# Optimization experiments

Hardware: AMD Instinct MI355X
Metric: run time of the kernel (lower is better)

Reference implementation:

```python
import jax, jax.numpy as jnp
import numpy as np

NEG_SLOPE = 0.2   # opt.alpha for LeakyReLU
NEG_INF = -9e15   # mask fill used by LocalAggregator

B, L, D, V = 512, 100, 128, 200000


def setup_inputs() -> dict:
    key = jax.random.key(0)
    ks = jax.random.split(key, 6)
    stdv = 1.0 / np.sqrt(D)
    inputs = jax.random.randint(ks[0], (B, L), 0, V)
    adj = jax.random.randint(ks[1], (B, L, L), 0, 5)        # edge types 0..4
    mask_item = jax.random.randint(ks[2], (B, L), 0, 2)
    item = jax.random.randint(ks[3], (B, L), 0, V)
    emb_table = jax.random.uniform(ks[4], (V, D), jnp.float32, -stdv, stdv)
    ka = jax.random.split(ks[5], 4)
    a0, a1, a2, a3 = [jax.random.uniform(k, (D,), jnp.float32, -stdv, stdv) for k in ka]
    return dict(inputs=inputs, adj=adj, mask_item=mask_item, item=item,
                emb_table=emb_table, a0=a0, a1=a1, a2=a2, a3=a3)


def reference(inputs, adj, mask_item, item, emb_table, a0, a1, a2, a3):
    # h = self.embedding(inputs)
    h = emb_table[inputs]  # [B, L, D]

    # LocalAggregator (GCE-GNN): a_input[b,i,j,:] = h[b,i,:] * h[b,j,:]
    # e_k = leakyrelu(a_input @ a_k); computed as a fused einsum (no BxLxLxD tensor)
    def att(a):
        return jax.nn.leaky_relu(jnp.einsum('bid,bjd,d->bij', h, h, a), NEG_SLOPE)

    e0, e1, e2, e3 = att(a0), att(a1), att(a2), att(a3)

    # select attention logit by edge type; non-edges masked to -9e15
    alpha = jnp.full_like(e0, NEG_INF)
    alpha = jnp.where(adj == 1, e0, alpha)
    alpha = jnp.where(adj == 2, e1, alpha)
    alpha = jnp.where(adj == 3, e2, alpha)
    alpha = jnp.where(adj == 4, e3, alpha)
    alpha = jax.nn.softmax(alpha, axis=-1)

    # output = alpha @ h (local aggregation); forward returns h_local
    return jnp.einsum('bij,bjd->bid', alpha, h)
```

## Files before the change

### kernel.cpp

```cpp
#include <hip/hip_runtime.h>
#include <hip/hip_bf16.h>

#define B_  512
#define L_  100
#define D_  128
#define SP_ 136
#define SO_ 132

typedef unsigned short ushort_t;
typedef __attribute__((ext_vector_type(8))) unsigned short us8;
typedef __attribute__((ext_vector_type(8))) __bf16 bf8;
typedef __attribute__((ext_vector_type(4))) float f4;
typedef __attribute__((ext_vector_type(4))) float f4v;
typedef __attribute__((ext_vector_type(4))) int i4v;
typedef __attribute__((ext_vector_type(4))) unsigned int ui4;

__device__ __forceinline__ float b2f(ushort_t u) {
  union { unsigned i; float f; } v; v.i = ((unsigned)u) << 16; return v.f;
}
__device__ __forceinline__ ushort_t f2b(float f) {
  unsigned u = __float_as_uint(f);
  u += 0x7fffu + ((u >> 16) & 1u);
  return (ushort_t)(u >> 16);
}
__device__ __forceinline__ us8 pack8(const float* x) {
  union { __hip_bfloat162 h; unsigned u; } cv;
  ui4 pk;
#pragma unroll
  for (int t = 0; t < 4; ++t) {
    cv.h = __float22bfloat162_rn(make_float2(x[2 * t], x[2 * t + 1]));
    pk[t] = cv.u;
  }
  return __builtin_bit_cast(us8, pk);
}
__device__ __forceinline__ int sw(int row, int col) {
  return row * 128 + ((((col >> 3) ^ row) & 15) << 3) + (col & 7);
}
__device__ __forceinline__ int swT(int d, int col) {
  int mix = (d & 15) ^ ((d >> 3) & 15);
  return d * 128 + ((((col >> 3) ^ mix) & 15) << 3) + (col & 7);
}

__global__ __launch_bounds__(448, 4)
void CombineGraph_fused(const int* __restrict__ inp, const int* __restrict__ adjG,
                        const float* __restrict__ embF,
                        const float* __restrict__ a0F, const float* __restrict__ a1F,
                        const float* __restrict__ a2F, const float* __restrict__ a3F,
                        float* __restrict__ outG) {
  __shared__ __align__(16) unsigned char smem[77584];
  ushort_t* Hs = (ushort_t*)smem;
  ushort_t* HsT = (ushort_t*)(smem + 32768);
  unsigned char* adjS = smem + 65536;
  float* aVf = (float*)(smem + 75536);

  const int b = blockIdx.x, tid = threadIdx.x;
  const int w = tid / 64, lane = tid & 63, c = lane & 15, q = lane >> 4;
  const int mi = w;

  int idxv[5];
#pragma unroll
  for (int it = 0; it < 5; ++it) {
    int u = tid + it * 448;
    int r = u >> 4;
    idxv[it] = (u < 2048 && r < L_) ? inp[b * L_ + r] : 0;
  }

  i4v av[6];
#pragma unroll
  for (int it = 0; it < 6; ++it) {
    int u = tid + it * 448;
    if (u < 2500) av[it] = *(const i4v*)(adjG + (size_t)b * 10000 + u * 4);
  }

  for (int u = tid; u < 512; u += 448) {
    int k = u >> 7, d = u & 127;
    const float* ak = (k == 0) ? a0F : (k == 1) ? a1F : (k == 2) ? a2F : a3F;
    aVf[u] = ak[d];
  }

#pragma unroll
  for (int it = 0; it < 6; ++it) {
    int u = tid + it * 448;
    if (u < 2500) {
      i4v v = av[it];
      unsigned pk = (unsigned)(v[0] & 255) | ((unsigned)(v[1] & 255) << 8) |
                    ((unsigned)(v[2] & 255) << 16) | ((unsigned)(v[3] & 255) << 24);
      *(unsigned*)&adjS[u * 4] = pk;
    }
  }
  __builtin_amdgcn_sched_barrier(0);

  f4v ev0[5], ev1[5];
#pragma unroll
  for (int it = 0; it < 5; ++it) {
    int u = tid + it * 448;
    int r = u >> 4, ch = u & 15;
    if (u < 2048 && r < L_) {
      const float* src = embF + ((size_t)idxv[it] << 7) + ch * 8;
      ev0[it] = *(const f4v*)src;
      ev1[it] = *(const f4v*)(src + 4);
    }
  }
#pragma unroll
  for (int it = 0; it < 5; ++it) {
    int u = tid + it * 448;
    if (u < 2048) {
      int r = u >> 4, ch = u & 15;
      us8 o = {0, 0, 0, 0, 0, 0, 0, 0};
      if (r < L_) {
        float x[8];
#pragma unroll
        for (int t = 0; t < 4; ++t) { x[t] = ev0[it][t]; x[4 + t] = ev1[it][t]; }
        o = pack8(x);
      }
      *(us8*)&Hs[sw(r, ch * 8)] = o;
#pragma unroll
      for (int t = 0; t < 8; ++t)
        HsT[swT(ch * 8 + t, r)] = o[t];
    }
  }
  __syncthreads();

  unsigned tpk[7];
#pragma unroll
  for (int nt = 0; nt < 7; ++nt) {
    int j = nt * 16 + c;
    int jc = (j < L_) ? j : L_ - 1;
    unsigned pk = 0;
#pragma unroll
    for (int r4 = 0; r4 < 4; ++r4) {
      int i = mi * 16 + q * 4 + r4;
      int t = adjS[(i < L_ ? i : L_ - 1) * 100 + jc];
      t = (i < L_ && j < L_) ? t : 0;
      pk |= ((unsigned)t) << (8 * r4);
    }
    tpk[nt] = pk;
  }

  float lg[7][4];
#pragma unroll
  for (int nt = 0; nt < 7; ++nt)
#pragma unroll
    for (int r4 = 0; r4 < 4; ++r4) lg[nt][r4] = -9e15f;

#pragma unroll
  for (int k = 0; k < 4; ++k) {
    us8 Afk[4];
#pragma unroll
    for (int ks = 0; ks < 4; ++ks) {
      us8 hr = *(const us8*)&Hs[sw(mi * 16 + c, ks * 32 + q * 8)];
      const float* ap = &aVf[k * 128 + ks * 32 + q * 8];
      f4v av0 = *(const f4v*)ap;
      f4v av1 = *(const f4v*)(ap + 4);
      float pr[8];
#pragma unroll
      for (int t = 0; t < 4; ++t) {
        pr[t]     = b2f(hr[t])     * av0[t];
        pr[4 + t] = b2f(hr[4 + t]) * av1[t];
      }
      Afk[ks] = pack8(pr);
    }
#pragma unroll
    for (int nt = 0; nt < 7; ++nt) {
      f4 acc = {0, 0, 0, 0};
#pragma unroll
      for (int ks = 0; ks < 4; ++ks) {
        bf8 bb = __builtin_bit_cast(bf8, *(const us8*)&Hs[sw(nt * 16 + c, ks * 32 + q * 8)]);
        acc = __builtin_amdgcn_mfma_f32_16x16x32_bf16(__builtin_bit_cast(bf8, Afk[ks]), bb, acc, 0, 0, 0);
      }
#pragma unroll
      for (int r4 = 0; r4 < 4; ++r4) {
        int t = (int)((tpk[nt] >> (8 * r4)) & 255u);
        float e = acc[r4];
        e = (e > 0.f) ? e : 0.2f * e;
        lg[nt][r4] = (t == k + 1) ? e : lg[nt][r4];
      }
    }
    __builtin_amdgcn_sched_barrier(0);
  }

  __syncthreads();

  ushort_t* Pw = (ushort_t*)smem + w * 16 * SP_;
#pragma unroll
  for (int r4 = 0; r4 < 4; ++r4) {
    float m = lg[0][r4];
#pragma unroll
    for (int nt = 1; nt < 7; ++nt) m = fmaxf(m, lg[nt][r4]);
#pragma unroll
    for (int off = 1; off <= 8; off <<= 1) m = fmaxf(m, __shfl_xor(m, off, 64));
    float ex[7], s = 0.f;
#pragma unroll
    for (int nt = 0; nt < 7; ++nt) { ex[nt] = __expf(lg[nt][r4] - m); s += ex[nt]; }
#pragma unroll
    for (int off = 1; off <= 8; off <<= 1) s += __shfl_xor(s, off, 64);
    float inv = 1.0f / s;
    int row = q * 4 + r4;
#pragma unroll
    for (int nt = 0; nt < 7; ++nt) Pw[row * SP_ + nt * 16 + c] = f2b(ex[nt] * inv);
  }
#pragma unroll
  for (int t = 0; t < 4; ++t) Pw[c * SP_ + 112 + q * 4 + t] = 0;

  asm volatile("s_waitcnt lgkmcnt(0)" ::: "memory");
  __builtin_amdgcn_sched_barrier(0);

  us8 Pf[4];
#pragma unroll
  for (int ks = 0; ks < 4; ++ks)
    Pf[ks] = *(const us8*)&Pw[c * SP_ + ks * 32 + q * 8];
  f4 oc[8];
#pragma unroll
  for (int nt2 = 0; nt2 < 8; ++nt2) {
    f4 a = {0, 0, 0, 0};
#pragma unroll
    for (int ks = 0; ks < 4; ++ks) {
      bf8 ob = __builtin_bit_cast(bf8, *(const us8*)&HsT[swT(nt2 * 16 + c, ks * 32 + q * 8)]);
      a = __builtin_amdgcn_mfma_f32_16x16x32_bf16(__builtin_bit_cast(bf8, Pf[ks]), ob, a, 0, 0, 0);
    }
    oc[nt2] = a;
  }
  __syncthreads();

  float* Ot = (float*)smem;
#pragma unroll
  for (int nt2 = 0; nt2 < 8; ++nt2)
#pragma unroll
    for (int r4 = 0; r4 < 4; ++r4)
      Ot[(w * 16 + q * 4 + r4) * SO_ + nt2 * 16 + c] = oc[nt2][r4];
#pragma unroll
  for (int it = 0; it < 8; ++it) {
    int u = it * 64 + lane;
    int row16 = u >> 5, col4 = u & 31;
    int i = w * 16 + row16;
    if (i < L_) {
      f4 vv = *(const f4*)&Ot[(w * 16 + row16) * SO_ + col4 * 4];
      *(f4*)&outG[((size_t)b * L_ + i) * D_ + col4 * 4] = vv;
    }
  }
}

extern "C" void kernel_launch(void* const* d_in, const int* in_sizes, int n_in,
                              void* d_out, int out_size, void* d_ws, size_t ws_size,
                              hipStream_t stream) {
  (void)d_ws; (void)ws_size; (void)out_size;
  const int* inp = nullptr; const int* adj = nullptr;
  const float* emb = nullptr; const float* aP[4] = {nullptr, nullptr, nullptr, nullptr};
  int na = 0;
  for (int i = 0; i < n_in; ++i) {
    int s = in_sizes[i];
    if (s == 25600000)            emb = (const float*)d_in[i];
    else if (s == 5120000)        adj = (const int*)d_in[i];
    else if (s == 128 && na < 4)  aP[na++] = (const float*)d_in[i];
    else if (s == 51200 && !inp)  inp = (const int*)d_in[i];
  }
  CombineGraph_fused<<<dim3(B_), dim3(448), 0, stream>>>(
      inp, adj, emb, aP[0], aP[1], aP[2], aP[3], (float*)d_out);
}
```

Before: 186.5 us.

## Read adjacency directly into registers, drop LDS staging, add setprio around MFMA

```diff
diff --git a/kernel.cpp b/kernel.cpp
--- a/kernel.cpp
+++ b/kernel.cpp
@@ -5,14 +5,11 @@
 #define L_  100
 #define D_  128
 #define SP_ 136
-#define SO_ 132
-
 typedef unsigned short ushort_t;
 typedef __attribute__((ext_vector_type(8))) unsigned short us8;
 typedef __attribute__((ext_vector_type(8))) __bf16 bf8;
 typedef __attribute__((ext_vector_type(4))) float f4;
 typedef __attribute__((ext_vector_type(4))) float f4v;
-typedef __attribute__((ext_vector_type(4))) int i4v;
 typedef __attribute__((ext_vector_type(4))) unsigned int ui4;
 
 __device__ __forceinline__ float b2f(ushort_t u) {
@@ -47,11 +44,10 @@
                         const float* __restrict__ a0F, const float* __restrict__ a1F,
                         const float* __restrict__ a2F, const float* __restrict__ a3F,
                         float* __restrict__ outG) {
-  __shared__ __align__(16) unsigned char smem[77584];
+  __shared__ __align__(16) unsigned char smem[67584];
   ushort_t* Hs = (ushort_t*)smem;
   ushort_t* HsT = (ushort_t*)(smem + 32768);
-  unsigned char* adjS = smem + 65536;
-  float* aVf = (float*)(smem + 75536);
+  float* aVf = (float*)(smem + 65536);
 
   const int b = blockIdx.x, tid = threadIdx.x;
   const int w = tid / 64, lane = tid & 63, c = lane & 15, q = lane >> 4;
@@ -65,28 +61,29 @@
     idxv[it] = (u < 2048 && r < L_) ? inp[b * L_ + r] : 0;
   }
 
-  i4v av[6];
-#pragma unroll
-  for (int it = 0; it < 6; ++it) {
-    int u = tid + it * 448;
-    if (u < 2500) av[it] = *(const i4v*)(adjG + (size_t)b * 10000 + u * 4);
-  }
-
-  for (int u = tid; u < 512; u += 448) {
-    int k = u >> 7, d = u & 127;
+  unsigned tpk[7];
+#pragma unroll
+  for (int nt = 0; nt < 7; ++nt) {
+    int j = nt * 16 + c;
+    int jc = (j < L_) ? j : L_ - 1;
+    unsigned pk = 0;
+#pragma unroll
+    for (int r4 = 0; r4 < 4; ++r4) {
+      int i = mi * 16 + q * 4 + r4;
+      int ic = (i < L_) ? i : L_ - 1;
+      int t = adjG[(size_t)b * 10000 + ic * 100 + jc];
+      t = (i < L_ && j < L_) ? t : 0;
+      pk |= ((unsigned)t) << (8 * r4);
+    }
+    tpk[nt] = pk;
+  }
+
+  {
+    int k = tid >> 7, d = tid & 127;
     const float* ak = (k == 0) ? a0F : (k == 1) ? a1F : (k == 2) ? a2F : a3F;
-    aVf[u] = ak[d];
-  }
-
-#pragma unroll
-  for (int it = 0; it < 6; ++it) {
-    int u = tid + it * 448;
-    if (u < 2500) {
-      i4v v = av[it];
-      unsigned pk = (unsigned)(v[0] & 255) | ((unsigned)(v[1] & 255) << 8) |
-                    ((unsigned)(v[2] & 255) << 16) | ((unsigned)(v[3] & 255) << 24);
-      *(unsigned*)&adjS[u * 4] = pk;
-    }
+    aVf[tid] = ak[d];
+    int u2 = tid + 448;
+    if (u2 < 512) aVf[u2] = a3F[u2 & 127];
   }
   __builtin_amdgcn_sched_barrier(0);
 
@@ -113,29 +110,13 @@
         for (int t = 0; t < 4; ++t) { x[t] = ev0[it][t]; x[4 + t] = ev1[it][t]; }
         o = pack8(x);
       }
-      *(us8*)&Hs[sw(r, ch * 8)] = o;
+      if (r < 112) *(us8*)&Hs[sw(r, ch * 8)] = o;
 #pragma unroll
       for (int t = 0; t < 8; ++t)
         HsT[swT(ch * 8 + t, r)] = o[t];
     }
   }
   __syncthreads();
-
-  unsigned tpk[7];
-#pragma unroll
-  for (int nt = 0; nt < 7; ++nt) {
-    int j = nt * 16 + c;
-    int jc = (j < L_) ? j : L_ - 1;
-    unsigned pk = 0;
-#pragma unroll
-    for (int r4 = 0; r4 < 4; ++r4) {
-      int i = mi * 16 + q * 4 + r4;
-      int t = adjS[(i < L_ ? i : L_ - 1) * 100 + jc];
-      t = (i < L_ && j < L_) ? t : 0;
-      pk |= ((unsigned)t) << (8 * r4);
-    }
-    tpk[nt] = pk;
-  }
 
   float lg[7][4];
 #pragma unroll
@@ -160,6 +141,7 @@
       }
       Afk[ks] = pack8(pr);
     }
+    __builtin_amdgcn_s_setprio(1);
 #pragma unroll
     for (int nt = 0; nt < 7; ++nt) {
       f4 acc = {0, 0, 0, 0};
@@ -176,6 +158,7 @@
         lg[nt][r4] = (t == k + 1) ? e : lg[nt][r4];
       }
     }
+    __builtin_amdgcn_s_setprio(0);
     __builtin_amdgcn_sched_barrier(0);
   }
 
@@ -210,6 +193,7 @@
   for (int ks = 0; ks < 4; ++ks)
     Pf[ks] = *(const us8*)&Pw[c * SP_ + ks * 32 + q * 8];
   f4 oc[8];
+  __builtin_amdgcn_s_setprio(1);
 #pragma unroll
   for (int nt2 = 0; nt2 < 8; ++nt2) {
     f4 a = {0, 0, 0, 0};
@@ -220,22 +204,16 @@
     }
     oc[nt2] = a;
   }
-  __syncthreads();
-
-  float* Ot = (float*)smem;
-#pragma unroll
-  for (int nt2 = 0; nt2 < 8; ++nt2)
-#pragma unroll
-    for (int r4 = 0; r4 < 4; ++r4)
-      Ot[(w * 16 + q * 4 + r4) * SO_ + nt2 * 16 + c] = oc[nt2][r4];
-#pragma unroll
-  for (int it = 0; it < 8; ++it) {
-    int u = it * 64 + lane;
-    int row16 = u >> 5, col4 = u & 31;
-    int i = w * 16 + row16;
+  __builtin_amdgcn_s_setprio(0);
+
+#pragma unroll
+  for (int r4 = 0; r4 < 4; ++r4) {
+    int i = w * 16 + q * 4 + r4;
     if (i < L_) {
-      f4 vv = *(const f4*)&Ot[(w * 16 + row16) * SO_ + col4 * 4];
-      *(f4*)&outG[((size_t)b * L_ + i) * D_ + col4 * 4] = vv;
+      float* dst = outG + ((size_t)b * L_ + i) * D_ + c;
+#pragma unroll
+      for (int nt2 = 0; nt2 < 8; ++nt2)
+        dst[nt2 * 16] = oc[nt2][r4];
     }
   }
 }
```

Result: no change. 184.3 us (-1.2%).
